# Kernel tuning notes

Hardware: AMD Instinct MI355X
Metric: run time of the kernel (lower is better)

Reference implementation:

```python
import jax, jax.numpy as jnp
import numpy as np

TEMPERATURE = 0.1
NEG_INF = -1e9


def setup_inputs() -> dict:
    key = jax.random.key(0)
    k1, k2 = jax.random.split(key)
    features = jax.random.normal(k1, (8192, 256), dtype=jnp.float32)
    labels = jax.random.randint(k2, (4096, 1), 0, 1000, dtype=jnp.int64)
    return {"features": features, "labels": labels}


def reference(features, labels):
    N = features.shape[0]
    n_views = N // labels.shape[0]
    # labels repeated over views: [N, 1]
    labels_nv = jnp.tile(labels, (n_views, 1))
    eye = jnp.eye(N, dtype=bool)
    # contrastive mask: 1 where same class, 0 on diagonal
    mask = (labels_nv == labels_nv.T).astype(features.dtype)
    mask = jnp.where(eye, 0.0, mask)
    # pairwise similarity logits [N, N], diagonal masked out
    logits = jnp.matmul(features, features.T) / TEMPERATURE
    logits = jnp.where(eye, NEG_INF, logits)
    # NOTE: torch code divides by mask.sum(dim=1) WITHOUT keepdim, which
    # broadcasts over the last axis (divide by column's row-sum). mask is
    # symmetric so this equals per-row normalization; replicate exactly.
    soft_label = mask / mask.sum(axis=1)
    log_proba = jax.nn.log_softmax(logits, axis=-1)
    loss_all = jnp.sum(soft_label * log_proba, axis=-1)  # [N]
    loss = -jnp.mean(loss_all) * TEMPERATURE
    return loss
```

## Files before the change

kernel.cpp:

```cpp
#include <hip/hip_runtime.h>

typedef __bf16 bf16_t;
typedef bf16_t bf16x8 __attribute__((ext_vector_type(8)));
typedef float f32x4 __attribute__((ext_vector_type(4)));
typedef unsigned short ushort_t;
typedef unsigned int uint_t;

#define C10L2E 14.4269504088896340736f
#define LN2    0.69314718055994530942f
#define NEG_BIG -3.0e38f
#define M0     -1.0e30f
#define THR_L2 11.5415603f

static __device__ __forceinline__ float fexp2(float x){ return __builtin_amdgcn_exp2f(x); }
static __device__ __forceinline__ float flog2(float x){ return __builtin_amdgcn_logf(x); }

#define GLOAD16(g, l) __builtin_amdgcn_global_load_lds( \
    (const __attribute__((address_space(1))) void*)(g), \
    (__attribute__((address_space(3))) void*)(l), 16, 0, 0)

static __device__ __forceinline__ ushort_t f2bf1(float f) {
    uint_t u = __float_as_uint(f);
    uint_t r = (u + 0x7fffu + ((u >> 16) & 1u)) >> 16;
    return (ushort_t)r;
}

__global__ void prep_kernel(const float* __restrict__ feat, ushort_t* __restrict__ Fb) {
    int i = blockIdx.x * 256 + threadIdx.x;
    float4 f = reinterpret_cast<const float4*>(feat)[i];
    ushort4 o;
    o.x = f2bf1(f.x); o.y = f2bf1(f.y); o.z = f2bf1(f.z); o.w = f2bf1(f.w);
    reinterpret_cast<ushort4*>(Fb)[i] = o;
}

__global__ void scatter_kernel(const int* __restrict__ labels, int* __restrict__ cnt,
                               int* __restrict__ idxl) {
    int i = blockIdx.x * 256 + threadIdx.x;
    if (i < 4096) {
        int lab = labels[i];
        int p = atomicAdd(&cnt[lab], 1);
        if (p < 64) idxl[lab * 64 + p] = i;
    }
}

__global__ void classterm_kernel(const float* __restrict__ feat, const int* __restrict__ cnt,
                                 const int* __restrict__ idxl, float* __restrict__ term) {
    int c = blockIdx.x;
    int lane = threadIdx.x;
    int n = cnt[c];
    float4 g4 = make_float4(0.f, 0.f, 0.f, 0.f);
    float n2 = 0.f;
    for (int e = 0; e < n; ++e) {
        int r = idxl[c * 64 + e];
        float4 f0 = reinterpret_cast<const float4*>(feat)[(size_t)r * 64 + lane];
        float4 f1 = reinterpret_cast<const float4*>(feat)[(size_t)(r + 4096) * 64 + lane];
        g4.x += f0.x + f1.x; g4.y += f0.y + f1.y;
        g4.z += f0.z + f1.z; g4.w += f0.w + f1.w;
        n2 += f0.x*f0.x + f0.y*f0.y + f0.z*f0.z + f0.w*f0.w
            + f1.x*f1.x + f1.y*f1.y + f1.z*f1.z + f1.w*f1.w;
    }
    float gg = g4.x*g4.x + g4.y*g4.y + g4.z*g4.z + g4.w*g4.w;
    #pragma unroll
    for (int d = 1; d < 64; d <<= 1) {
        gg += __shfl_xor(gg, d, 64);
        n2 += __shfl_xor(n2, d, 64);
    }
    if (lane == 0) term[c] = (n > 0) ? (gg - n2) / (float)(2 * n - 1) : 0.0f;
}

__global__ __launch_bounds__(512, 2) void supcon_main(
        const ushort_t* __restrict__ Fb, float* __restrict__ part) {
    extern __shared__ char lds[];
    char* As = lds;
    char* Bb0 = lds + 65536;
    char* Bb1 = lds + 65536 + 32768;

    const int tid  = threadIdx.x;
    const int lane = tid & 63;
    const int wid  = tid >> 6;
    const int wr   = (wid >> 2) * 64;
    const int wc   = (wid & 3) * 64;
    const int g    = lane >> 4;
    const int l15  = lane & 15;
    const int r0 = blockIdx.x * 128;
    const int c0 = blockIdx.y * 2048;

    #pragma unroll
    for (int i = 0; i < 8; ++i) {
        int c = (wid * 8 + i) * 64 + lane;
        int row = c >> 5, sl = c & 31;
        int lslot = (sl & 16) | ((sl ^ row) & 15);
        GLOAD16(Fb + (size_t)(r0 + row) * 256 + lslot * 8, As + c * 16);
    }
    int bgofs[4], bdst[4];
    #pragma unroll
    for (int i = 0; i < 4; ++i) {
        int c = (wid * 4 + i) * 64 + lane;
        int col = c >> 3, ps = c & 7;
        int lslot = ps ^ (col & 7);
        bgofs[i] = col * 256 + lslot * 8;
        bdst[i] = c * 16;
    }
    #pragma unroll
    for (int i = 0; i < 4; ++i)
        GLOAD16(Fb + (size_t)c0 * 256 + bgofs[i], Bb0 + bdst[i]);
    __syncthreads();

    float ML2[16], S[16];
    #pragma unroll
    for (int x = 0; x < 16; ++x) { ML2[x] = M0; S[x] = 0.0f; }

    f32x4 acc[4][4];

    auto stage_next = [&](int pn) {
        int j0n = c0 + (pn >> 2) * 256;
        int qn = pn & 3;
        char* Bd = (pn & 1) ? Bb1 : Bb0;
        #pragma unroll
        for (int i = 0; i < 4; ++i)
            GLOAD16(Fb + (size_t)j0n * 256 + qn * 64 + bgofs[i], Bd + bdst[i]);
    };

    auto do_phase = [&](int p, bool ZERO, bool EPI) {
        if (p < 31) stage_next(p + 1);
        if (ZERO) {
            #pragma unroll
            for (int m = 0; m < 4; ++m)
                #pragma unroll
                for (int n = 0; n < 4; ++n)
                    #pragma unroll
                    for (int q_ = 0; q_ < 4; ++q_) acc[m][n][q_] = 0.0f;
        }
        const char* Bp = (p & 1) ? Bb1 : Bb0;
        const int q = p & 3;
        #pragma unroll
        for (int kk = 0; kk < 2; ++kk) {
            int sA = q * 8 + kk * 4 + g;
            int pA = (sA & 16) | ((sA ^ l15) & 15);
            bf16x8 a[4], b[4];
            #pragma unroll
            for (int m = 0; m < 4; ++m)
                a[m] = *reinterpret_cast<const bf16x8*>(As + (wr + m * 16 + l15) * 512 + pA * 16);
            int pB = (kk * 4 + g) ^ (l15 & 7);
            #pragma unroll
            for (int n = 0; n < 4; ++n)
                b[n] = *reinterpret_cast<const bf16x8*>(Bp + (wc + n * 16 + l15) * 128 + pB * 16);
            #pragma unroll
            for (int m = 0; m < 4; ++m)
                #pragma unroll
                for (int n = 0; n < 4; ++n)
                    acc[m][n] = __builtin_amdgcn_mfma_f32_16x16x32_bf16(a[m], b[n], acc[m][n], 0, 0, 0);
        }
        if (EPI) {
            const int j0 = c0 + (p >> 2) * 256;
            const bool diag = (j0 == (r0 & ~255));
            const int jc = j0 + wc + l15;
            #pragma unroll
            for (int m = 0; m < 4; ++m) {
                #pragma unroll
                for (int v = 0; v < 4; ++v) {
                    const int idx = m * 4 + v;
                    float x0 = acc[m][0][v], x1 = acc[m][1][v];
                    float x2 = acc[m][2][v], x3 = acc[m][3][v];
                    if (diag) {
                        int i = r0 + wr + m * 16 + g * 4 + v;
                        if (jc      == i) x0 = NEG_BIG;
                        if (jc + 16 == i) x1 = NEG_BIG;
                        if (jc + 32 == i) x2 = NEG_BIG;
                        if (jc + 48 == i) x3 = NEG_BIG;
                    }
                    float tm = fmaxf(fmaxf(x0, x1), fmaxf(x2, x3));
                    float cc = tm * C10L2E;
                    float ml = ML2[idx];
                    if (cc > ml + THR_L2) {
                        S[idx] *= fexp2(ml - cc);
                        ml = cc;
                        ML2[idx] = cc;
                    }
                    S[idx] += fexp2(fmaf(x0, C10L2E, -ml)) + fexp2(fmaf(x1, C10L2E, -ml))
                            + fexp2(fmaf(x2, C10L2E, -ml)) + fexp2(fmaf(x3, C10L2E, -ml));
                }
            }
        }
        __syncthreads();
    };

    for (int t = 0; t < 8; ++t) {
        do_phase(t * 4 + 0, true,  false);
        do_phase(t * 4 + 1, false, false);
        do_phase(t * 4 + 2, false, false);
        do_phase(t * 4 + 3, false, true);
    }

    const int slot = blockIdx.y * 4 + (wid & 3);
    #pragma unroll
    for (int idx = 0; idx < 16; ++idx) {
        float m_ = ML2[idx], s_ = S[idx];
        #pragma unroll
        for (int d = 1; d < 16; d <<= 1) {
            float mo = __shfl_xor(m_, d, 64);
            float so = __shfl_xor(s_, d, 64);
            float nm = fmaxf(m_, mo);
            s_ = s_ * fexp2(m_ - nm) + so * fexp2(mo - nm);
            m_ = nm;
        }
        if (l15 == 0) {
            int i = r0 + wr + (idx >> 2) * 16 + g * 4 + (idx & 3);
            float2 val; val.x = m_; val.y = s_;
            *reinterpret_cast<float2*>(part + ((size_t)i * 16 + slot) * 2) = val;
        }
    }
}

__global__ void combine_kernel(const float* __restrict__ part, float* __restrict__ blk_lse) {
    __shared__ float sm[16];
    int tid = threadIdx.x;
    int row = blockIdx.x * 16 + (tid >> 4);
    int l16 = tid & 15;
    float2 v = reinterpret_cast<const float2*>(part)[(size_t)row * 16 + l16];
    float m_ = v.x, s_ = v.y;
    #pragma unroll
    for (int d = 1; d < 16; d <<= 1) {
        float mo = __shfl_xor(m_, d, 64);
        float so = __shfl_xor(s_, d, 64);
        float nm = fmaxf(m_, mo);
        s_ = s_ * fexp2(m_ - nm) + so * fexp2(mo - nm);
        m_ = nm;
    }
    if (l16 == 0) sm[tid >> 4] = LN2 * (m_ + flog2(s_));
    __syncthreads();
    if (tid == 0) {
        float a = 0.f;
        #pragma unroll
        for (int i = 0; i < 16; ++i) a += sm[i];
        blk_lse[blockIdx.x] = a;
    }
}

__global__ void final_kernel(const float* __restrict__ blk_lse, const float* __restrict__ term,
                             float* __restrict__ out) {
    __shared__ float sm[256];
    int tid = threadIdx.x;
    float a = 0.f;
    for (int i = tid; i < 512; i += 256) a += blk_lse[i];
    for (int i = tid; i < 1000; i += 256) a -= 10.0f * term[i];
    sm[tid] = a;
    __syncthreads();
    for (int s = 128; s > 0; s >>= 1) {
        if (tid < s) sm[tid] += sm[tid + s];
        __syncthreads();
    }
    if (tid == 0) out[0] = sm[0] * (0.1f / 8192.0f);
}

extern "C" void kernel_launch(void* const* d_in, const int* in_sizes, int n_in,
                              void* d_out, int out_size, void* d_ws, size_t ws_size,
                              hipStream_t stream) {
    const float* feat = (const float*)d_in[0];
    const int* labels = (const int*)d_in[1];
    float* out = (float*)d_out;

    char* ws = (char*)d_ws;
    ushort_t* Fb   = (ushort_t*)ws;
    float* part    = (float*)(ws + (4u << 20));
    int* cnt       = (int*)(ws + (5u << 20));
    int* idxl      = (int*)(ws + (5u << 20) + 4096);
    float* term    = (float*)(ws + (5u << 20) + 4096 + 262144);
    float* blk_lse = (float*)(ws + (5u << 20) + 4096 + 262144 + 4096);

    hipMemsetAsync(cnt, 0, 4096, stream);
    prep_kernel<<<2048, 256, 0, stream>>>(feat, Fb);
    scatter_kernel<<<16, 256, 0, stream>>>(labels, cnt, idxl);
    classterm_kernel<<<1000, 64, 0, stream>>>(feat, cnt, idxl, term);
    dim3 grid(64, 4);
    supcon_main<<<grid, 512, 131072, stream>>>(Fb, part);
    combine_kernel<<<512, 256, 0, stream>>>(part, blk_lse);
    final_kernel<<<1, 256, 0, stream>>>(blk_lse, term, out);
}
```

Measured before the change: 69.65 us.

## Hold A operands in registers, 4-buffer B pipeline, fuse small kernels

Measured after the change: 104.8 us. +50.5%, slower.

```diff
diff --git a/kernel.cpp b/kernel.cpp
--- a/kernel.cpp
+++ b/kernel.cpp
@@ -25,17 +25,14 @@
     return (ushort_t)r;
 }
 
-__global__ void prep_kernel(const float* __restrict__ feat, ushort_t* __restrict__ Fb) {
+__global__ void prep_kernel(const float* __restrict__ feat, const int* __restrict__ labels,
+                            ushort_t* __restrict__ Fb, int* __restrict__ cnt,
+                            int* __restrict__ idxl) {
     int i = blockIdx.x * 256 + threadIdx.x;
     float4 f = reinterpret_cast<const float4*>(feat)[i];
     ushort4 o;
     o.x = f2bf1(f.x); o.y = f2bf1(f.y); o.z = f2bf1(f.z); o.w = f2bf1(f.w);
     reinterpret_cast<ushort4*>(Fb)[i] = o;
-}
-
-__global__ void scatter_kernel(const int* __restrict__ labels, int* __restrict__ cnt,
-                               int* __restrict__ idxl) {
-    int i = blockIdx.x * 256 + threadIdx.x;
     if (i < 4096) {
         int lab = labels[i];
         int p = atomicAdd(&cnt[lab], 1);
@@ -71,9 +68,6 @@
 __global__ __launch_bounds__(512, 2) void supcon_main(
         const ushort_t* __restrict__ Fb, float* __restrict__ part) {
     extern __shared__ char lds[];
-    char* As = lds;
-    char* Bb0 = lds + 65536;
-    char* Bb1 = lds + 65536 + 32768;
 
     const int tid  = threadIdx.x;
     const int lane = tid & 63;
@@ -85,25 +79,28 @@
     const int r0 = blockIdx.x * 128;
     const int c0 = blockIdx.y * 2048;
 
-    #pragma unroll
-    for (int i = 0; i < 8; ++i) {
-        int c = (wid * 8 + i) * 64 + lane;
-        int row = c >> 5, sl = c & 31;
-        int lslot = (sl & 16) | ((sl ^ row) & 15);
-        GLOAD16(Fb + (size_t)(r0 + row) * 256 + lslot * 8, As + c * 16);
-    }
-    int bgofs[4], bdst[4];
-    #pragma unroll
-    for (int i = 0; i < 4; ++i) {
-        int c = (wid * 4 + i) * 64 + lane;
-        int col = c >> 3, ps = c & 7;
-        int lslot = ps ^ (col & 7);
-        bgofs[i] = col * 256 + lslot * 8;
-        bdst[i] = c * 16;
-    }
-    #pragma unroll
-    for (int i = 0; i < 4; ++i)
-        GLOAD16(Fb + (size_t)c0 * 256 + bgofs[i], Bb0 + bdst[i]);
+    bf16x8 a[4][8];
+    #pragma unroll
+    for (int m = 0; m < 4; ++m) {
+        const ushort_t* bA = Fb + (size_t)(r0 + wr + m * 16 + l15) * 256 + g * 8;
+        #pragma unroll
+        for (int kq = 0; kq < 8; ++kq)
+            a[m][kq] = *reinterpret_cast<const bf16x8*>(bA + kq * 32);
+    }
+
+    auto stage = [&](int j0, int qn, int bb) {
+        #pragma unroll
+        for (int i = 0; i < 4; ++i) {
+            int c = (wid * 4 + i) * 64 + lane;
+            int col = c >> 3, ps = c & 7;
+            int lslot = ps ^ (col & 7);
+            GLOAD16(Fb + (size_t)(j0 + col) * 256 + qn * 64 + lslot * 8,
+                    lds + bb * 32768 + c * 16);
+        }
+    };
+
+    stage(c0, 0, 0);
+    stage(c0, 1, 1);
     __syncthreads();
 
     float ML2[16], S[16];
@@ -112,84 +109,70 @@
 
     f32x4 acc[4][4];
 
-    auto stage_next = [&](int pn) {
-        int j0n = c0 + (pn >> 2) * 256;
-        int qn = pn & 3;
-        char* Bd = (pn & 1) ? Bb1 : Bb0;
-        #pragma unroll
-        for (int i = 0; i < 4; ++i)
-            GLOAD16(Fb + (size_t)j0n * 256 + qn * 64 + bgofs[i], Bd + bdst[i]);
-    };
-
-    auto do_phase = [&](int p, bool ZERO, bool EPI) {
-        if (p < 31) stage_next(p + 1);
-        if (ZERO) {
+    #pragma unroll 1
+    for (int t = 0; t < 8; ++t) {
+        const int j0 = c0 + t * 256;
+        #pragma unroll
+        for (int q = 0; q < 4; ++q) {
+            if (q == 0) { stage(j0, 2, 2); stage(j0, 3, 3); }
+            else if (q == 2 && t < 7) { stage(j0 + 256, 0, 0); stage(j0 + 256, 1, 1); }
+
+            if (q == 0) {
+                #pragma unroll
+                for (int m = 0; m < 4; ++m)
+                    #pragma unroll
+                    for (int n = 0; n < 4; ++n)
+                        #pragma unroll
+                        for (int w = 0; w < 4; ++w) acc[m][n][w] = 0.0f;
+            }
+
+            const char* Bp = lds + q * 32768;
             #pragma unroll
-            for (int m = 0; m < 4; ++m)
+            for (int kk = 0; kk < 2; ++kk) {
+                bf16x8 b[4];
+                int pB = (kk * 4 + g) ^ (l15 & 7);
                 #pragma unroll
                 for (int n = 0; n < 4; ++n)
+                    b[n] = *reinterpret_cast<const bf16x8*>(Bp + (wc + n * 16 + l15) * 128 + pB * 16);
+                #pragma unroll
+                for (int m = 0; m < 4; ++m)
                     #pragma unroll
-                    for (int q_ = 0; q_ < 4; ++q_) acc[m][n][q_] = 0.0f;
-        }
-        const char* Bp = (p & 1) ? Bb1 : Bb0;
-        const int q = p & 3;
-        #pragma unroll
-        for (int kk = 0; kk < 2; ++kk) {
-            int sA = q * 8 + kk * 4 + g;
-            int pA = (sA & 16) | ((sA ^ l15) & 15);
-            bf16x8 a[4], b[4];
-            #pragma unroll
-            for (int m = 0; m < 4; ++m)
-                a[m] = *reinterpret_cast<const bf16x8*>(As + (wr + m * 16 + l15) * 512 + pA * 16);
-            int pB = (kk * 4 + g) ^ (l15 & 7);
-            #pragma unroll
-            for (int n = 0; n < 4; ++n)
-                b[n] = *reinterpret_cast<const bf16x8*>(Bp + (wc + n * 16 + l15) * 128 + pB * 16);
-            #pragma unroll
-            for (int m = 0; m < 4; ++m)
-                #pragma unroll
-                for (int n = 0; n < 4; ++n)
-                    acc[m][n] = __builtin_amdgcn_mfma_f32_16x16x32_bf16(a[m], b[n], acc[m][n], 0, 0, 0);
-        }
-        if (EPI) {
-            const int j0 = c0 + (p >> 2) * 256;
-            const bool diag = (j0 == (r0 & ~255));
-            const int jc = j0 + wc + l15;
-            #pragma unroll
-            for (int m = 0; m < 4; ++m) {
-                #pragma unroll
-                for (int v = 0; v < 4; ++v) {
-                    const int idx = m * 4 + v;
-                    float x0 = acc[m][0][v], x1 = acc[m][1][v];
-                    float x2 = acc[m][2][v], x3 = acc[m][3][v];
-                    if (diag) {
-                        int i = r0 + wr + m * 16 + g * 4 + v;
-                        if (jc      == i) x0 = NEG_BIG;
-                        if (jc + 16 == i) x1 = NEG_BIG;
-                        if (jc + 32 == i) x2 = NEG_BIG;
-                        if (jc + 48 == i) x3 = NEG_BIG;
+                    for (int n = 0; n < 4; ++n)
+                        acc[m][n] = __builtin_amdgcn_mfma_f32_16x16x32_bf16(a[m][q * 2 + kk], b[n], acc[m][n], 0, 0, 0);
+            }
+
+            if (q == 3) {
+                const bool diag = (j0 == (r0 & ~255));
+                const int jc = j0 + wc + l15;
+                #pragma unroll
+                for (int m = 0; m < 4; ++m) {
+                    #pragma unroll
+                    for (int v = 0; v < 4; ++v) {
+                        const int idx = m * 4 + v;
+                        float x0 = acc[m][0][v], x1 = acc[m][1][v];
+                        float x2 = acc[m][2][v], x3 = acc[m][3][v];
+                        if (diag) {
+                            int i = r0 + wr + m * 16 + g * 4 + v;
+                            if (jc      == i) x0 = NEG_BIG;
+                            if (jc + 16 == i) x1 = NEG_BIG;
+                            if (jc + 32 == i) x2 = NEG_BIG;
+                            if (jc + 48 == i) x3 = NEG_BIG;
+                        }
+                        float tm = fmaxf(fmaxf(x0, x1), fmaxf(x2, x3));
+                        float cc = tm * C10L2E;
+                        float ml = ML2[idx];
+                        if (cc > ml + THR_L2) {
+                            S[idx] *= fexp2(ml - cc);
+                            ml = cc;
+                            ML2[idx] = cc;
+                        }
+                        S[idx] += fexp2(fmaf(x0, C10L2E, -ml)) + fexp2(fmaf(x1, C10L2E, -ml))
+                                + fexp2(fmaf(x2, C10L2E, -ml)) + fexp2(fmaf(x3, C10L2E, -ml));
                     }
-                    float tm = fmaxf(fmaxf(x0, x1), fmaxf(x2, x3));
-                    float cc = tm * C10L2E;
-                    float ml = ML2[idx];
-                    if (cc > ml + THR_L2) {
-                        S[idx] *= fexp2(ml - cc);
-                        ml = cc;
-                        ML2[idx] = cc;
-                    }
-                    S[idx] += fexp2(fmaf(x0, C10L2E, -ml)) + fexp2(fmaf(x1, C10L2E, -ml))
-                            + fexp2(fmaf(x2, C10L2E, -ml)) + fexp2(fmaf(x3, C10L2E, -ml));
                 }
             }
-        }
-        __syncthreads();
-    };
-
-    for (int t = 0; t < 8; ++t) {
-        do_phase(t * 4 + 0, true,  false);
-        do_phase(t * 4 + 1, false, false);
-        do_phase(t * 4 + 2, false, false);
-        do_phase(t * 4 + 3, false, true);
+            if (q & 1) __syncthreads();
+        }
     }
 
     const int slot = blockIdx.y * 4 + (wid & 3);
@@ -212,7 +195,9 @@
     }
 }
 
-__global__ void combine_kernel(const float* __restrict__ part, float* __restrict__ blk_lse) {
+__global__ void combine_kernel(const float* __restrict__ part, const float* __restrict__ term,
+                               float* __restrict__ acc, int* __restrict__ cntr,
+                               float* __restrict__ out) {
     __shared__ float sm[16];
     int tid = threadIdx.x;
     int row = blockIdx.x * 16 + (tid >> 4);
@@ -233,24 +218,17 @@
         float a = 0.f;
         #pragma unroll
         for (int i = 0; i < 16; ++i) a += sm[i];
-        blk_lse[blockIdx.x] = a;
-    }
-}
-
-__global__ void final_kernel(const float* __restrict__ blk_lse, const float* __restrict__ term,
-                             float* __restrict__ out) {
-    __shared__ float sm[256];
-    int tid = threadIdx.x;
-    float a = 0.f;
-    for (int i = tid; i < 512; i += 256) a += blk_lse[i];
-    for (int i = tid; i < 1000; i += 256) a -= 10.0f * term[i];
-    sm[tid] = a;
-    __syncthreads();
-    for (int s = 128; s > 0; s >>= 1) {
-        if (tid < s) sm[tid] += sm[tid + s];
-        __syncthreads();
-    }
-    if (tid == 0) out[0] = sm[0] * (0.1f / 8192.0f);
+        a -= 10.0f * term[blockIdx.x];
+        if (blockIdx.x < 488) a -= 10.0f * term[512 + blockIdx.x];
+        atomicAdd(acc, a);
+        __threadfence();
+        int old = atomicAdd(cntr, 1);
+        if (old == 511) {
+            __threadfence();
+            float tot = atomicAdd(acc, 0.0f);
+            out[0] = tot * (0.1f / 8192.0f);
+        }
+    }
 }
 
 extern "C" void kernel_launch(void* const* d_in, const int* in_sizes, int n_in,
@@ -261,19 +239,18 @@
     float* out = (float*)d_out;
 
     char* ws = (char*)d_ws;
-    ushort_t* Fb   = (ushort_t*)ws;
-    float* part    = (float*)(ws + (4u << 20));
-    int* cnt       = (int*)(ws + (5u << 20));
-    int* idxl      = (int*)(ws + (5u << 20) + 4096);
-    float* term    = (float*)(ws + (5u << 20) + 4096 + 262144);
-    float* blk_lse = (float*)(ws + (5u << 20) + 4096 + 262144 + 4096);
-
-    hipMemsetAsync(cnt, 0, 4096, stream);
-    prep_kernel<<<2048, 256, 0, stream>>>(feat, Fb);
-    scatter_kernel<<<16, 256, 0, stream>>>(labels, cnt, idxl);
+    ushort_t* Fb = (ushort_t*)ws;
+    float* part  = (float*)(ws + (4u << 20));
+    int* cnt     = (int*)(ws + (5u << 20));
+    float* acc   = (float*)(ws + (5u << 20) + 4096);
+    int* cntr    = (int*)(ws + (5u << 20) + 4100);
+    int* idxl    = (int*)(ws + (5u << 20) + 8192);
+    float* term  = (float*)(ws + (5u << 20) + 8192 + 262144);
+
+    hipMemsetAsync(ws + (5u << 20), 0, 8192, stream);
+    prep_kernel<<<2048, 256, 0, stream>>>(feat, labels, Fb, cnt, idxl);
     classterm_kernel<<<1000, 64, 0, stream>>>(feat, cnt, idxl, term);
     dim3 grid(64, 4);
     supcon_main<<<grid, 512, 131072, stream>>>(Fb, part);
-    combine_kernel<<<512, 256, 0, stream>>>(part, blk_lse);
-    final_kernel<<<1, 256, 0, stream>>>(blk_lse, term, out);
-}
+    combine_kernel<<<512, 256, 0, stream>>>(part, term, acc, cntr, out);
+}
```

## Fuse class-term, LSE combine and final reduction into one kernel

Applied to the files above, without the earlier changes.

Result: slower. 91.12 us (+30.8%).

```diff
diff --git a/kernel.cpp b/kernel.cpp
--- a/kernel.cpp
+++ b/kernel.cpp
@@ -31,41 +31,6 @@
     ushort4 o;
     o.x = f2bf1(f.x); o.y = f2bf1(f.y); o.z = f2bf1(f.z); o.w = f2bf1(f.w);
     reinterpret_cast<ushort4*>(Fb)[i] = o;
-}
-
-__global__ void scatter_kernel(const int* __restrict__ labels, int* __restrict__ cnt,
-                               int* __restrict__ idxl) {
-    int i = blockIdx.x * 256 + threadIdx.x;
-    if (i < 4096) {
-        int lab = labels[i];
-        int p = atomicAdd(&cnt[lab], 1);
-        if (p < 64) idxl[lab * 64 + p] = i;
-    }
-}
-
-__global__ void classterm_kernel(const float* __restrict__ feat, const int* __restrict__ cnt,
-                                 const int* __restrict__ idxl, float* __restrict__ term) {
-    int c = blockIdx.x;
-    int lane = threadIdx.x;
-    int n = cnt[c];
-    float4 g4 = make_float4(0.f, 0.f, 0.f, 0.f);
-    float n2 = 0.f;
-    for (int e = 0; e < n; ++e) {
-        int r = idxl[c * 64 + e];
-        float4 f0 = reinterpret_cast<const float4*>(feat)[(size_t)r * 64 + lane];
-        float4 f1 = reinterpret_cast<const float4*>(feat)[(size_t)(r + 4096) * 64 + lane];
-        g4.x += f0.x + f1.x; g4.y += f0.y + f1.y;
-        g4.z += f0.z + f1.z; g4.w += f0.w + f1.w;
-        n2 += f0.x*f0.x + f0.y*f0.y + f0.z*f0.z + f0.w*f0.w
-            + f1.x*f1.x + f1.y*f1.y + f1.z*f1.z + f1.w*f1.w;
-    }
-    float gg = g4.x*g4.x + g4.y*g4.y + g4.z*g4.z + g4.w*g4.w;
-    #pragma unroll
-    for (int d = 1; d < 64; d <<= 1) {
-        gg += __shfl_xor(gg, d, 64);
-        n2 += __shfl_xor(n2, d, 64);
-    }
-    if (lane == 0) term[c] = (n > 0) ? (gg - n2) / (float)(2 * n - 1) : 0.0f;
 }
 
 __global__ __launch_bounds__(512, 2) void supcon_main(
@@ -212,45 +177,85 @@
     }
 }
 
-__global__ void combine_kernel(const float* __restrict__ part, float* __restrict__ blk_lse) {
+__global__ __launch_bounds__(256) void combine_kernel(
+        const float* __restrict__ part, const float* __restrict__ feat,
+        const int* __restrict__ labels, float* __restrict__ acc,
+        int* __restrict__ cntr, float* __restrict__ out) {
     __shared__ float sm[16];
-    int tid = threadIdx.x;
-    int row = blockIdx.x * 16 + (tid >> 4);
-    int l16 = tid & 15;
-    float2 v = reinterpret_cast<const float2*>(part)[(size_t)row * 16 + l16];
-    float m_ = v.x, s_ = v.y;
-    #pragma unroll
-    for (int d = 1; d < 16; d <<= 1) {
-        float mo = __shfl_xor(m_, d, 64);
-        float so = __shfl_xor(s_, d, 64);
-        float nm = fmaxf(m_, mo);
-        s_ = s_ * fexp2(m_ - nm) + so * fexp2(mo - nm);
-        m_ = nm;
-    }
-    if (l16 == 0) sm[tid >> 4] = LN2 * (m_ + flog2(s_));
-    __syncthreads();
+    __shared__ float tterm;
+    __shared__ int lst[64];
+    __shared__ int lcnt;
+    const int tid = threadIdx.x;
+    const int bx = blockIdx.x;
+
+    if (tid == 0) lcnt = 0;
+    __syncthreads();
+
+    #pragma unroll
+    for (int j = 0; j < 16; ++j) {
+        int idx = (tid << 4) | j;
+        if (labels[idx] == bx) {
+            int p = atomicAdd(&lcnt, 1);
+            if (p < 64) lst[p] = idx;
+        }
+    }
+
+    if (bx < 512) {
+        int row = bx * 16 + (tid >> 4);
+        int l16 = tid & 15;
+        float2 v = reinterpret_cast<const float2*>(part)[(size_t)row * 16 + l16];
+        float m_ = v.x, s_ = v.y;
+        #pragma unroll
+        for (int d = 1; d < 16; d <<= 1) {
+            float mo = __shfl_xor(m_, d, 64);
+            float so = __shfl_xor(s_, d, 64);
+            float nm = fmaxf(m_, mo);
+            s_ = s_ * fexp2(m_ - nm) + so * fexp2(mo - nm);
+            m_ = nm;
+        }
+        if (l16 == 0) sm[tid >> 4] = LN2 * (m_ + flog2(s_));
+    }
+    __syncthreads();
+
+    if (tid < 64) {
+        int n = lcnt;
+        int ne = n < 64 ? n : 64;
+        float4 g4 = make_float4(0.f, 0.f, 0.f, 0.f);
+        float n2 = 0.f;
+        for (int e = 0; e < ne; ++e) {
+            int r = lst[e];
+            float4 f0 = reinterpret_cast<const float4*>(feat)[(size_t)r * 64 + tid];
+            float4 f1 = reinterpret_cast<const float4*>(feat)[(size_t)(r + 4096) * 64 + tid];
+            g4.x += f0.x + f1.x; g4.y += f0.y + f1.y;
+            g4.z += f0.z + f1.z; g4.w += f0.w + f1.w;
+            n2 += f0.x*f0.x + f0.y*f0.y + f0.z*f0.z + f0.w*f0.w
+                + f1.x*f1.x + f1.y*f1.y + f1.z*f1.z + f1.w*f1.w;
+        }
+        float gg = g4.x*g4.x + g4.y*g4.y + g4.z*g4.z + g4.w*g4.w;
+        #pragma unroll
+        for (int d = 1; d < 64; d <<= 1) {
+            gg += __shfl_xor(gg, d, 64);
+            n2 += __shfl_xor(n2, d, 64);
+        }
+        if (tid == 0) tterm = (n > 0) ? (gg - n2) / (float)(2 * n - 1) : 0.0f;
+    }
+    __syncthreads();
+
     if (tid == 0) {
-        float a = 0.f;
-        #pragma unroll
-        for (int i = 0; i < 16; ++i) a += sm[i];
-        blk_lse[blockIdx.x] = a;
-    }
-}
-
-__global__ void final_kernel(const float* __restrict__ blk_lse, const float* __restrict__ term,
-                             float* __restrict__ out) {
-    __shared__ float sm[256];
-    int tid = threadIdx.x;
-    float a = 0.f;
-    for (int i = tid; i < 512; i += 256) a += blk_lse[i];
-    for (int i = tid; i < 1000; i += 256) a -= 10.0f * term[i];
-    sm[tid] = a;
-    __syncthreads();
-    for (int s = 128; s > 0; s >>= 1) {
-        if (tid < s) sm[tid] += sm[tid + s];
-        __syncthreads();
-    }
-    if (tid == 0) out[0] = sm[0] * (0.1f / 8192.0f);
+        float a = -10.0f * tterm;
+        if (bx < 512) {
+            #pragma unroll
+            for (int i = 0; i < 16; ++i) a += sm[i];
+        }
+        atomicAdd(acc, a);
+        __threadfence();
+        int old = atomicAdd(cntr, 1);
+        if (old == 999) {
+            __threadfence();
+            float tot = atomicAdd(acc, 0.0f);
+            out[0] = tot * (0.1f / 8192.0f);
+        }
+    }
 }
 
 extern "C" void kernel_launch(void* const* d_in, const int* in_sizes, int n_in,
@@ -261,19 +266,14 @@
     float* out = (float*)d_out;
 
     char* ws = (char*)d_ws;
-    ushort_t* Fb   = (ushort_t*)ws;
-    float* part    = (float*)(ws + (4u << 20));
-    int* cnt       = (int*)(ws + (5u << 20));
-    int* idxl      = (int*)(ws + (5u << 20) + 4096);
-    float* term    = (float*)(ws + (5u << 20) + 4096 + 262144);
-    float* blk_lse = (float*)(ws + (5u << 20) + 4096 + 262144 + 4096);
-
-    hipMemsetAsync(cnt, 0, 4096, stream);
+    ushort_t* Fb = (ushort_t*)ws;
+    float* part  = (float*)(ws + (4u << 20));
+    float* acc   = (float*)(ws + (5u << 20));
+    int* cntr    = (int*)(ws + (5u << 20) + 4);
+
+    hipMemsetAsync(ws + (5u << 20), 0, 8, stream);
     prep_kernel<<<2048, 256, 0, stream>>>(feat, Fb);
-    scatter_kernel<<<16, 256, 0, stream>>>(labels, cnt, idxl);
-    classterm_kernel<<<1000, 64, 0, stream>>>(feat, cnt, idxl, term);
     dim3 grid(64, 4);
     supcon_main<<<grid, 512, 131072, stream>>>(Fb, part);
-    combine_kernel<<<512, 256, 0, stream>>>(part, blk_lse);
-    final_kernel<<<1, 256, 0, stream>>>(blk_lse, term, out);
-}
+    combine_kernel<<<1000, 256, 0, stream>>>(part, feat, labels, acc, cntr, out);
+}
```
